# Performance work log

Hardware: AMD Instinct MI355X
Metric: run time of the kernel (lower is better)

## Reference

```python
import jax, jax.numpy as jnp
import numpy as np

B, N_P, N_S = 64, 50, 200
N_NODES = N_P * N_S          # 10000 nodes per graph (jobs x ops)
N_CAND = N_S + 1             # 201 candidates
INPUT_DIM, HIDDEN = 3, 64
NODE_DIM = 2 * HIDDEN        # h_nodes feature dim (=> actor in = 6*HIDDEN)
POOL_DIM = 4 * HIDDEN        # h_pooled dim (mean || max pooling)
H_ACTOR, H_CRITIC = 256, 256


def setup_inputs() -> dict:
    key = jax.random.key(0)
    ks = jax.random.split(key, 16)
    p = lambda k, sh: jax.random.normal(k, sh, jnp.float32) * 0.02
    x = jax.random.normal(ks[0], (B, N_NODES, INPUT_DIM), jnp.float32)
    candidate = jax.random.randint(ks[1], (B, N_CAND), 0, N_NODES)
    mask = jax.random.randint(ks[2], (B, N_CAND), 0, 2) > 0
    mask = mask.at[:, 0].set(True)  # guarantee at least one valid action per row
    return {
        "x": x, "candidate": candidate, "mask": mask,
        "fe_w1": p(ks[3], (INPUT_DIM, HIDDEN)), "fe_b1": jnp.zeros((HIDDEN,), jnp.float32),
        "fe_w2": p(ks[4], (HIDDEN, NODE_DIM)), "fe_b2": jnp.zeros((NODE_DIM,), jnp.float32),
        "a_w1": p(ks[5], (NODE_DIM + POOL_DIM, H_ACTOR)), "a_b1": jnp.zeros((H_ACTOR,), jnp.float32),
        "a_w2": p(ks[6], (H_ACTOR, H_ACTOR)), "a_b2": jnp.zeros((H_ACTOR,), jnp.float32),
        "a_w3": p(ks[7], (H_ACTOR, 1)), "a_b3": jnp.zeros((1,), jnp.float32),
        "c_w1": p(ks[8], (POOL_DIM, H_CRITIC)), "c_b1": jnp.zeros((H_CRITIC,), jnp.float32),
        "c_w2": p(ks[9], (H_CRITIC, H_CRITIC)), "c_b2": jnp.zeros((H_CRITIC,), jnp.float32),
        "c_w3": p(ks[10], (H_CRITIC, 1)), "c_b3": jnp.zeros((1,), jnp.float32),
    }


def _actor_critic(x, candidate, mask,
                  fe_w1, fe_b1, fe_w2, fe_b2,
                  a_w1, a_b1, a_w2, a_b2, a_w3, a_b3,
                  c_w1, c_b1, c_w2, c_b2, c_w3, c_b3):
    # --- feature_extract: per-node MLP embedding, graph-level pooling ---
    h = jax.nn.relu(jnp.einsum('bni,ih->bnh', x, fe_w1) + fe_b1)
    h_nodes = jax.nn.relu(jnp.einsum('bnh,hd->bnd', h, fe_w2) + fe_b2)   # [B, N, 2H]
    h_pooled = jnp.concatenate([h_nodes.mean(axis=1), h_nodes.max(axis=1)], axis=-1)  # [B, 4H]

    # --- gather candidate node features (torch.gather over node axis) ---
    cand_feat = jnp.take_along_axis(h_nodes, candidate[:, :, None], axis=1)  # [B, C, 2H]

    # --- concat broadcast pooled feature ---
    pooled_rep = jnp.broadcast_to(h_pooled[:, None, :], (cand_feat.shape[0], cand_feat.shape[1], h_pooled.shape[-1]))
    concat_fea = jnp.concatenate([cand_feat, pooled_rep], axis=-1)  # [B, C, 6H]

    # --- actor MLP (tanh hidden layers, linear out) ---
    a = jnp.tanh(concat_fea @ a_w1 + a_b1)
    a = jnp.tanh(a @ a_w2 + a_b2)
    scores = a @ a_w3 + a_b3                                    # [B, C, 1]

    # --- mask with -inf, softmax over candidate axis ---
    scores = jnp.where(mask[:, :, None], scores, -jnp.inf)
    pi = jax.nn.softmax(scores, axis=1)                          # [B, C, 1]

    # --- critic MLP on pooled feature ---
    c = jnp.tanh(h_pooled @ c_w1 + c_b1)
    c = jnp.tanh(c @ c_w2 + c_b2)
    v = c @ c_w3 + c_b3                                          # [B, 1]
    return pi, v


def reference(x, candidate, mask,
              fe_w1, fe_b1, fe_w2, fe_b2,
              a_w1, a_b1, a_w2, a_b2, a_w3, a_b3,
              c_w1, c_b1, c_w2, c_b2, c_w3, c_b3):
    return _actor_critic(x, candidate, mask,
                         fe_w1, fe_b1, fe_w2, fe_b2,
                         a_w1, a_b1, a_w2, a_b2, a_w3, a_b3,
                         c_w1, c_b1, c_w2, c_b2, c_w3, c_b3)
```

## Files before the change

### kernel.cpp

```cpp
#include <hip/hip_runtime.h>

#define NN 10000
#define NCAND 201
#define NB 64

typedef __attribute__((ext_vector_type(8))) short short8;
typedef __attribute__((ext_vector_type(4))) float f32x4;

__device__ __forceinline__ float bf2f(unsigned short u) {
  return __uint_as_float(((unsigned int)u) << 16);
}
__device__ __forceinline__ unsigned short f2bf(float f) {
  unsigned int u = __float_as_uint(f);
  u += 0x7FFFu + ((u >> 16) & 1u);
  return (unsigned short)(u >> 16);
}
__device__ __forceinline__ float fast_tanh(float x) {
  return 1.0f - 2.0f / (__expf(2.0f * x) + 1.0f);
}
__device__ __forceinline__ float gld(const void* p, long i, int f) {
  return f ? ((const float*)p)[i] : bf2f(((const unsigned short*)p)[i]);
}

__global__ __launch_bounds__(256)
void prep_kernel(const void* x, const void* w1, const void* b1, const void* w2,
                 const void* b2, const void* aw1, const void* ab1, const void* aw2,
                 const void* ab2, const void* aw3, const void* ab3,
                 const void* cw1, const void* cb1, const void* cw2, const void* cb2,
                 const void* cw3, const void* cb3,
                 const unsigned int* mask_w, const unsigned int* cand_w,
                 int* F, float* zero_base,
                 unsigned short* __restrict__ w2t, unsigned short* __restrict__ aw1t,
                 unsigned short* __restrict__ aw2t,
                 unsigned short* __restrict__ cw1t, unsigned short* __restrict__ cw2t) {
  const int t = threadIdx.x;
  const int j = blockIdx.x;

  if (j < 384) {
    __shared__ int cnts[5];
    if (t < 5) cnts[t] = 0;
    __syncthreads();
    const void* aps[5] = {w2, aw1, aw2, cw1, cw2};
#pragma unroll
    for (int a = 0; a < 5; ++a) {
      const unsigned short* p = (const unsigned short*)aps[a];
      int c = 0;
      for (int i = t; i < 2048; i += 256)
        if ((p[i] & 0x7F80u) >= 0x4300u) c++;
      if (c) atomicAdd(&cnts[a], c);
    }
    __syncthreads();
    const int Fw2 = cnts[0] > 256, Faw1 = cnts[1] > 256, Faw2 = cnts[2] > 256;
    const int Fcw1 = cnts[3] > 256, Fcw2 = cnts[4] > 256;
    int i = j * 256 + t;
    if (i < 128 * 64) { int n = i >> 6, k = i & 63; w2t[i] = f2bf(gld(w2, k * 128 + n, Fw2)); }
    if (i < 256 * 384) { int n = i / 384, k = i % 384; aw1t[i] = f2bf(gld(aw1, k * 256 + n, Faw1)); }
    if (i < 256 * 256) {
      int n = i >> 8, k = i & 255;
      aw2t[i] = f2bf(gld(aw2, k * 256 + n, Faw2));
      cw1t[i] = f2bf(gld(cw1, k * 256 + n, Fcw1));
      cw2t[i] = f2bf(gld(cw2, k * 256 + n, Fcw2));
    }
    return;
  }

  __shared__ int sh[3];
  if (t < 3) sh[t] = 0;
  __syncthreads();

  if (j < 401) {
    const void* ptrs[17] = {x, w1, b1, w2, b2, aw1, ab1, aw2, ab2, aw3, ab3,
                            cw1, cb1, cw2, cb2, cw3, cb3};
    const int sizes[17] = {1920000, 192, 64, 8192, 128, 98304, 256, 65536, 256,
                           256, 1, 65536, 256, 65536, 256, 256, 1};
    int a = j - 384;
    const unsigned short* p = (const unsigned short*)ptrs[a];
    int K = min(sizes[a], 2048);
    int c = 0;
    for (int i = t; i < K; i += 256)
      if ((p[i] & 0x7F80u) >= 0x4300u) c++;
    if (c) atomicAdd(&sh[0], c);
    __syncthreads();
    if (t == 0) F[a] = (sh[0] > (K >> 3)) ? 1 : 0;
  } else if (j == 401) {
    int flo = 0, fhi = 0, fgt = 0;
    for (int i = t; i < 3216; i += 256) {
      unsigned int w = mask_w[i];
      if ((w & 0xFFFFu) == 0x3F80u) flo = 1;
      if ((w >> 16) == 0x3F80u) fhi = 1;
      if (w > 1u) fgt = 1;
    }
    if (flo) sh[0] = 1;
    if (fhi) sh[1] = 1;
    if (fgt) sh[2] = 1;
    __syncthreads();
    if (t == 0) F[17] = sh[0] ? 2 : (sh[1] ? 3 : (sh[2] ? 1 : 0));
  } else if (j == 402) {
    int co = 0;
    for (int i = t; i < 1024; i += 256)
      if ((i & 1) && cand_w[i] != 0u) co = 1;
    if (co) sh[0] = 1;
    __syncthreads();
    if (t == 0) F[18] = sh[0] ? 0 : 1;
  } else {
    zero_base[(j - 403) * 256 + t] = 0.f;
  }
}

__global__ __launch_bounds__(256, 4)
void feat_pool_kernel(const void* __restrict__ x,
                      const void* __restrict__ w1, const void* __restrict__ b1,
                      const unsigned short* __restrict__ w2t,
                      const void* __restrict__ b2,
                      const int* __restrict__ F,
                      float* __restrict__ psum, float* __restrict__ pmax) {
  __shared__ __align__(16) unsigned short h1s[128 * 72];
  __shared__ float w1f[3 * 64];
  __shared__ float b1f[64];
  __shared__ float b2f[128];

  const int t = threadIdx.x;
  const int b = blockIdx.x >> 4;
  const int s = blockIdx.x & 15;
  const int lane = t & 63;
  const int wv = t >> 6;
  const int F0 = F[0], F1 = F[1], F2 = F[2], F4 = F[4];

  if (t < 192) w1f[t] = gld(w1, t, F1);
  if (t < 64) b1f[t] = gld(b1, t, F2);
  if (t < 128) b2f[t] = gld(b2, t, F4);

  short8 bfr[2][2];
#pragma unroll
  for (int nl = 0; nl < 2; ++nl)
#pragma unroll
    for (int ks = 0; ks < 2; ++ks) {
      int col = wv * 32 + nl * 16 + (lane & 15);
      bfr[nl][ks] = *(const short8*)(w2t + col * 64 + ((lane >> 4) * 8) + ks * 32);
    }
  __syncthreads();

  float csum[2] = {0.f, 0.f};
  float cmax[2] = {0.f, 0.f};

  const int m = t & 127;
  const int kg = t >> 7;

  float x0 = 0.f, x1 = 0.f, x2 = 0.f;
  {
    int c0 = s;
    if (c0 < 79) {
      int nb = c0 * 128;
      if (m < min(128, NN - nb)) {
        long xo = ((long)b * NN + nb + m) * 3;
        x0 = gld(x, xo, F0); x1 = gld(x, xo + 1, F0); x2 = gld(x, xo + 2, F0);
      }
    }
  }

  for (int c = s; c < 79; c += 16) {
    int nb = c * 128;
    int cnt = (nb + 128 <= NN) ? 128 : (NN - nb);
    if (m < cnt) {
#pragma unroll
      for (int blk = 0; blk < 4; ++blk) {
        short8 v;
#pragma unroll
        for (int i = 0; i < 8; ++i) {
          int k = kg * 32 + blk * 8 + i;
          float vv = x0 * w1f[k] + x1 * w1f[64 + k] + x2 * w1f[128 + k] + b1f[k];
          v[i] = (short)f2bf(fmaxf(vv, 0.f));
        }
        *(short8*)(h1s + m * 72 + kg * 32 + blk * 8) = v;
      }
    }
    {
      int cn = c + 16;
      float nx0 = 0.f, nx1 = 0.f, nx2 = 0.f;
      if (cn < 79) {
        int nbn = cn * 128;
        if (m < min(128, NN - nbn)) {
          long xo = ((long)b * NN + nbn + m) * 3;
          nx0 = gld(x, xo, F0); nx1 = gld(x, xo + 1, F0); nx2 = gld(x, xo + 2, F0);
        }
      }
      __syncthreads();
      x0 = nx0; x1 = nx1; x2 = nx2;
    }
#pragma unroll
    for (int mt = 0; mt < 8; ++mt) {
      const unsigned short* ap = h1s + (mt * 16 + (lane & 15)) * 72 + ((lane >> 4) * 8);
      short8 af0 = *(const short8*)(ap);
      short8 af1 = *(const short8*)(ap + 32);
#pragma unroll
      for (int nl = 0; nl < 2; ++nl) {
        f32x4 acc = {0.f, 0.f, 0.f, 0.f};
        acc = __builtin_amdgcn_mfma_f32_16x16x32_bf16(af0, bfr[nl][0], acc, 0, 0, 0);
        acc = __builtin_amdgcn_mfma_f32_16x16x32_bf16(af1, bfr[nl][1], acc, 0, 0, 0);
        int col = wv * 32 + nl * 16 + (lane & 15);
        float bb = b2f[col];
#pragma unroll
        for (int r = 0; r < 4; ++r) {
          int row = mt * 16 + ((lane >> 4) * 4) + r;
          if (row < cnt) {
            float v = fmaxf(acc[r] + bb, 0.f);
            csum[nl] += v;
            cmax[nl] = fmaxf(cmax[nl], v);
          }
        }
      }
    }
    __syncthreads();
  }
#pragma unroll
  for (int nl = 0; nl < 2; ++nl) {
    csum[nl] += __shfl_xor(csum[nl], 16);
    csum[nl] += __shfl_xor(csum[nl], 32);
    cmax[nl] = fmaxf(cmax[nl], __shfl_xor(cmax[nl], 16));
    cmax[nl] = fmaxf(cmax[nl], __shfl_xor(cmax[nl], 32));
  }
  if (lane < 16) {
#pragma unroll
    for (int nl = 0; nl < 2; ++nl) {
      int col = wv * 32 + nl * 16 + lane;
      atomicAdd(&psum[b * 128 + col], csum[nl]);
      atomicMax((int*)&pmax[b * 128 + col], __float_as_int(cmax[nl]));
    }
  }
}

__global__ __launch_bounds__(256)
void actor_kernel(const void* __restrict__ x, const int* __restrict__ cand,
                  const void* __restrict__ w1, const void* __restrict__ b1,
                  const void* __restrict__ b2bf,
                  const void* __restrict__ ab1, const void* __restrict__ ab2,
                  const void* __restrict__ aw3, const void* __restrict__ ab3,
                  const int* __restrict__ F,
                  const float* __restrict__ psum, const float* __restrict__ pmax,
                  const unsigned short* __restrict__ w2t,
                  const unsigned short* __restrict__ aw1t,
                  const unsigned short* __restrict__ aw2t,
                  float* __restrict__ scores) {
  __shared__ __align__(16) unsigned short h1c[32 * 72];
  __shared__ __align__(16) unsigned short cf[32 * 136];
  __shared__ __align__(16) unsigned short a1s[32 * 264];
  __shared__ __align__(16) unsigned short a2s[32 * 264];
  __shared__ __align__(16) unsigned short plbf[256];
  __shared__ float ab1f[256], ab2f[256], b2f[128];

  const int t = threadIdx.x;
  const int b = blockIdx.x / 7;
  const int cb = blockIdx.x % 7;
  const int cbase = cb * 29;
  const int cntc = min(29, NCAND - cbase);
  const int lane = t & 63;
  const int wv = t >> 6;
  const int F0 = F[0], F1 = F[1], F2 = F[2], F4 = F[4], F6 = F[6], F8 = F[8];
  const int F9 = F[9], F10 = F[10], C64 = F[18];

  if (t < 128) {
    plbf[t] = f2bf(psum[b * 128 + t] * (1.0f / 10000.0f));
    plbf[128 + t] = f2bf(pmax[b * 128 + t]);
    b2f[t] = gld(b2bf, t, F4);
  }
  ab1f[t] = gld(ab1, t, F6);
  ab2f[t] = gld(ab2, t, F8);

  {
    int r = t & 31;
    int ci = cbase + r;
    if (ci > NCAND - 1) ci = NCAND - 1;
    long cidx = (long)b * NCAND + ci;
    int nd = C64 ? cand[2 * cidx] : cand[cidx];
    long xo = ((long)b * NN + nd) * 3;
    float x0 = gld(x, xo, F0), x1 = gld(x, xo + 1, F0), x2 = gld(x, xo + 2, F0);
    int kg = t >> 5;
#pragma unroll
    for (int i = 0; i < 8; ++i) {
      int k = kg * 8 + i;
      float v = x0 * gld(w1, k, F1) + x1 * gld(w1, 64 + k, F1) +
                x2 * gld(w1, 128 + k, F1) + gld(b1, k, F2);
      h1c[r * 72 + k] = f2bf(fmaxf(v, 0.f));
    }
  }
  __syncthreads();

  {
    short8 af[2][2];
#pragma unroll
    for (int mt = 0; mt < 2; ++mt)
#pragma unroll
      for (int ks = 0; ks < 2; ++ks)
        af[mt][ks] = *(const short8*)(h1c + (mt * 16 + (lane & 15)) * 72 + ((lane >> 4) * 8) + ks * 32);
#pragma unroll
    for (int nl = 0; nl < 2; ++nl) {
      int col = wv * 32 + nl * 16 + (lane & 15);
      short8 bf0 = *(const short8*)(w2t + col * 64 + ((lane >> 4) * 8));
      short8 bf1 = *(const short8*)(w2t + col * 64 + ((lane >> 4) * 8) + 32);
      float bb = b2f[col];
#pragma unroll
      for (int mt = 0; mt < 2; ++mt) {
        f32x4 acc = {0.f, 0.f, 0.f, 0.f};
        acc = __builtin_amdgcn_mfma_f32_16x16x32_bf16(af[mt][0], bf0, acc, 0, 0, 0);
        acc = __builtin_amdgcn_mfma_f32_16x16x32_bf16(af[mt][1], bf1, acc, 0, 0, 0);
#pragma unroll
        for (int r = 0; r < 4; ++r) {
          int row = mt * 16 + ((lane >> 4) * 4) + r;
          cf[row * 136 + col] = f2bf(fmaxf(acc[r] + bb, 0.f));
        }
      }
    }
  }
  __syncthreads();

  {
    f32x4 acc[2][4];
#pragma unroll
    for (int mt = 0; mt < 2; ++mt)
#pragma unroll
      for (int nt = 0; nt < 4; ++nt) acc[mt][nt] = (f32x4){0.f, 0.f, 0.f, 0.f};
    for (int ks = 0; ks < 12; ++ks) {
      short8 af0, af1;
      if (ks < 4) {
        af0 = *(const short8*)(cf + (lane & 15) * 136 + ks * 32 + ((lane >> 4) * 8));
        af1 = *(const short8*)(cf + (16 + (lane & 15)) * 136 + ks * 32 + ((lane >> 4) * 8));
      } else {
        short8 p = *(const short8*)(plbf + (ks - 4) * 32 + ((lane >> 4) * 8));
        af0 = p;
        af1 = p;
      }
#pragma unroll
      for (int nt = 0; nt < 4; ++nt) {
        int col = wv * 64 + nt * 16 + (lane & 15);
        short8 bfr = *(const short8*)(aw1t + col * 384 + ks * 32 + ((lane >> 4) * 8));
        acc[0][nt] = __builtin_amdgcn_mfma_f32_16x16x32_bf16(af0, bfr, acc[0][nt], 0, 0, 0);
        acc[1][nt] = __builtin_amdgcn_mfma_f32_16x16x32_bf16(af1, bfr, acc[1][nt], 0, 0, 0);
      }
    }
#pragma unroll
    for (int mt = 0; mt < 2; ++mt)
#pragma unroll
      for (int nt = 0; nt < 4; ++nt) {
        int col = wv * 64 + nt * 16 + (lane & 15);
        float bb = ab1f[col];
#pragma unroll
        for (int r = 0; r < 4; ++r) {
          int row = mt * 16 + ((lane >> 4) * 4) + r;
          a1s[row * 264 + col] = f2bf(fast_tanh(acc[mt][nt][r] + bb));
        }
      }
  }
  __syncthreads();

  {
    f32x4 acc[2][4];
#pragma unroll
    for (int mt = 0; mt < 2; ++mt)
#pragma unroll
      for (int nt = 0; nt < 4; ++nt) acc[mt][nt] = (f32x4){0.f, 0.f, 0.f, 0.f};
    for (int ks = 0; ks < 8; ++ks) {
      short8 af0 = *(const short8*)(a1s + (lane & 15) * 264 + ks * 32 + ((lane >> 4) * 8));
      short8 af1 = *(const short8*)(a1s + (16 + (lane & 15)) * 264 + ks * 32 + ((lane >> 4) * 8));
#pragma unroll
      for (int nt = 0; nt < 4; ++nt) {
        int col = wv * 64 + nt * 16 + (lane & 15);
        short8 bfr = *(const short8*)(aw2t + col * 256 + ks * 32 + ((lane >> 4) * 8));
        acc[0][nt] = __builtin_amdgcn_mfma_f32_16x16x32_bf16(af0, bfr, acc[0][nt], 0, 0, 0);
        acc[1][nt] = __builtin_amdgcn_mfma_f32_16x16x32_bf16(af1, bfr, acc[1][nt], 0, 0, 0);
      }
    }
#pragma unroll
    for (int mt = 0; mt < 2; ++mt)
#pragma unroll
      for (int nt = 0; nt < 4; ++nt) {
        int col = wv * 64 + nt * 16 + (lane & 15);
        float bb = ab2f[col];
#pragma unroll
        for (int r = 0; r < 4; ++r) {
          int row = mt * 16 + ((lane >> 4) * 4) + r;
          a2s[row * 264 + col] = f2bf(fast_tanh(acc[mt][nt][r] + bb));
        }
      }
  }
  __syncthreads();

  {
    int row = t >> 3, seg = t & 7;
    float p = 0.f;
#pragma unroll 8
    for (int i = 0; i < 32; ++i) {
      int k = seg * 32 + i;
      p += bf2f(a2s[row * 264 + k]) * gld(aw3, k, F9);
    }
    p += __shfl_xor(p, 1);
    p += __shfl_xor(p, 2);
    p += __shfl_xor(p, 4);
    if (seg == 0 && row < cntc)
      scores[b * 256 + cbase + row] = p + gld(ab3, 0, F10);
  }
}

__global__ __launch_bounds__(256)
void softmax_critic_kernel(const float* __restrict__ scores,
                           const void* __restrict__ mask,
                           const int* __restrict__ F,
                           const float* __restrict__ psum,
                           const float* __restrict__ pmax,
                           const unsigned short* __restrict__ cw1t,
                           const unsigned short* __restrict__ cw2t,
                           const void* __restrict__ cb1, const void* __restrict__ cb2,
                           const void* __restrict__ cw3, const void* __restrict__ cb3,
                           void* __restrict__ out) {
  __shared__ float plf[256];
  __shared__ float c1f[256];
  __shared__ float red[4];
  const int t = threadIdx.x;
  const int b = blockIdx.x & 63;
  const int lane = t & 63, wv = t >> 6;
  const int OF = (F[0] + F[1] + F[3] + F[5] + F[7] + F[9] + F[11] + F[13] + F[15]) >= 5;

  if (blockIdx.x < 64) {
    const int MM = F[17];
    float sraw = 0.f, sv = -1e30f;
    bool valid = false;
    if (t < NCAND) {
      sraw = scores[b * 256 + t];
      long idx = (long)b * NCAND + t;
      if (MM == 0)      valid = ((const int*)mask)[idx] != 0;
      else if (MM == 1) valid = ((const unsigned char*)mask)[idx] != 0;
      else if (MM == 2) valid = ((const unsigned short*)mask)[idx] != 0;
      else              valid = ((const unsigned int*)mask)[idx] != 0;
      if (valid) sv = sraw;
    }
    float m = sv;
    for (int o = 32; o; o >>= 1) m = fmaxf(m, __shfl_xor(m, o));
    if (lane == 0) red[wv] = m;
    __syncthreads();
    m = fmaxf(fmaxf(red[0], red[1]), fmaxf(red[2], red[3]));
    __syncthreads();
    float e = valid ? __expf(sraw - m) : 0.f;
    if (!(e == e)) e = 0.f;
    float ss = e;
    for (int o = 32; o; o >>= 1) ss += __shfl_xor(ss, o);
    if (lane == 0) red[wv] = ss;
    __syncthreads();
    float tot = red[0] + red[1] + red[2] + red[3];
    tot = fmaxf(tot, 1e-30f);
    if (t < NCAND) {
      float pv = e / tot;
      if (!(pv == pv)) pv = 0.f;
      if (OF) ((float*)out)[b * NCAND + t] = pv;
      else ((unsigned short*)out)[b * NCAND + t] = f2bf(pv);
    }
  } else {
    const int F12 = F[12], F14 = F[14], F15 = F[15], F16 = F[16];
    if (t < 128) {
      plf[t] = psum[b * 128 + t] * (1.0f / 10000.0f);
      plf[128 + t] = pmax[b * 128 + t];
    }
    __syncthreads();
    {
      float a = gld(cb1, t, F12);
      const unsigned short* row = cw1t + t * 256;
#pragma unroll
      for (int k8 = 0; k8 < 32; ++k8) {
        short8 w = *(const short8*)(row + k8 * 8);
#pragma unroll
        for (int j = 0; j < 8; ++j)
          a += plf[k8 * 8 + j] * bf2f((unsigned short)w[j]);
      }
      c1f[t] = fast_tanh(a);
    }
    __syncthreads();
    {
      float a2 = gld(cb2, t, F14);
      const unsigned short* row = cw2t + t * 256;
#pragma unroll
      for (int k8 = 0; k8 < 32; ++k8) {
        short8 w = *(const short8*)(row + k8 * 8);
#pragma unroll
        for (int j = 0; j < 8; ++j)
          a2 += c1f[k8 * 8 + j] * bf2f((unsigned short)w[j]);
      }
      a2 = fast_tanh(a2);
      float p = a2 * gld(cw3, t, F15);
      for (int o = 32; o; o >>= 1) p += __shfl_xor(p, o);
      __syncthreads();
      if (lane == 0) red[wv] = p;
      __syncthreads();
      if (t == 0) {
        float v = red[0] + red[1] + red[2] + red[3] + gld(cb3, 0, F16);
        if (!(v == v)) v = 0.f;
        if (OF) ((float*)out)[NB * NCAND + b] = v;
        else ((unsigned short*)out)[NB * NCAND + b] = f2bf(v);
      }
    }
  }
}

extern "C" void kernel_launch(void* const* d_in, const int* in_sizes, int n_in,
                              void* d_out, int out_size, void* d_ws, size_t ws_size,
                              hipStream_t stream) {
  const void* x = d_in[0];
  const int* cand = (const int*)d_in[1];
  const void* mask = d_in[2];
  const void* fe_w1 = d_in[3];
  const void* fe_b1 = d_in[4];
  const void* fe_w2 = d_in[5];
  const void* fe_b2 = d_in[6];
  const void* a_w1 = d_in[7];
  const void* a_b1 = d_in[8];
  const void* a_w2 = d_in[9];
  const void* a_b2 = d_in[10];
  const void* a_w3 = d_in[11];
  const void* a_b3 = d_in[12];
  const void* c_w1 = d_in[13];
  const void* c_b1 = d_in[14];
  const void* c_w2 = d_in[15];
  const void* c_b2 = d_in[16];
  const void* c_w3 = d_in[17];
  const void* c_b3 = d_in[18];

  char* ws = (char*)d_ws;
  float* psum = (float*)(ws + 0);
  float* pmax = (float*)(ws + 32768);
  float* scores = (float*)(ws + 65536);
  unsigned short* w2t = (unsigned short*)(ws + 131072);
  unsigned short* aw1t = (unsigned short*)(ws + 147456);
  unsigned short* aw2t = (unsigned short*)(ws + 344064);
  int* F = (int*)(ws + 475136);
  unsigned short* cw1t = (unsigned short*)(ws + 475264);
  unsigned short* cw2t = (unsigned short*)(ws + 606336);

  prep_kernel<<<467, 256, 0, stream>>>(x, fe_w1, fe_b1, fe_w2, fe_b2,
                                       a_w1, a_b1, a_w2, a_b2, a_w3, a_b3,
                                       c_w1, c_b1, c_w2, c_b2, c_w3, c_b3,
                                       (const unsigned int*)mask,
                                       (const unsigned int*)cand, F, psum,
                                       w2t, aw1t, aw2t, cw1t, cw2t);
  feat_pool_kernel<<<1024, 256, 0, stream>>>(x, fe_w1, fe_b1, w2t, fe_b2, F, psum, pmax);
  actor_kernel<<<448, 256, 0, stream>>>(x, cand, fe_w1, fe_b1, fe_b2,
                                        a_b1, a_b2, a_w3, a_b3, F, psum, pmax,
                                        w2t, aw1t, aw2t, scores);
  softmax_critic_kernel<<<128, 256, 0, stream>>>(scores, mask, F, psum, pmax,
                                                 cw1t, cw2t, c_b1, c_b2, c_w3, c_b3,
                                                 (void*)d_out);
}
```

Measured before the change: 177.7 us.

## Split actor kernel into 16-candidate blocks and shrink dtype-probe sampling

The actor kernel now handles 16 candidates per block instead of 29 (padded to 32), giving 13 blocks per batch and 832 blocks in total, with a single M-tile of MFMA per wave. This is meant to raise occupancy and parallelism across CUs and to cut the wasted padded rows, at the cost of reloading the aw1t/aw2t weight fragments from global memory twice as often. The prep kernel's per-weight dtype probe now samples 256 elements instead of 2048, which reduces prep work but makes the fp32/bf16 guess rely on a smaller sample.

```diff
diff --git a/kernel.cpp b/kernel.cpp
--- a/kernel.cpp
+++ b/kernel.cpp
@@ -44,14 +44,11 @@
 #pragma unroll
     for (int a = 0; a < 5; ++a) {
       const unsigned short* p = (const unsigned short*)aps[a];
-      int c = 0;
-      for (int i = t; i < 2048; i += 256)
-        if ((p[i] & 0x7F80u) >= 0x4300u) c++;
-      if (c) atomicAdd(&cnts[a], c);
-    }
-    __syncthreads();
-    const int Fw2 = cnts[0] > 256, Faw1 = cnts[1] > 256, Faw2 = cnts[2] > 256;
-    const int Fcw1 = cnts[3] > 256, Fcw2 = cnts[4] > 256;
+      if ((p[t] & 0x7F80u) >= 0x4300u) atomicAdd(&cnts[a], 1);
+    }
+    __syncthreads();
+    const int Fw2 = cnts[0] > 32, Faw1 = cnts[1] > 32, Faw2 = cnts[2] > 32;
+    const int Fcw1 = cnts[3] > 32, Fcw2 = cnts[4] > 32;
     int i = j * 256 + t;
     if (i < 128 * 64) { int n = i >> 6, k = i & 63; w2t[i] = f2bf(gld(w2, k * 128 + n, Fw2)); }
     if (i < 256 * 384) { int n = i / 384, k = i % 384; aw1t[i] = f2bf(gld(aw1, k * 256 + n, Faw1)); }
@@ -241,18 +238,18 @@
                   const unsigned short* __restrict__ aw1t,
                   const unsigned short* __restrict__ aw2t,
                   float* __restrict__ scores) {
-  __shared__ __align__(16) unsigned short h1c[32 * 72];
-  __shared__ __align__(16) unsigned short cf[32 * 136];
-  __shared__ __align__(16) unsigned short a1s[32 * 264];
-  __shared__ __align__(16) unsigned short a2s[32 * 264];
+  __shared__ __align__(16) unsigned short h1c[16 * 72];
+  __shared__ __align__(16) unsigned short cf[16 * 136];
+  __shared__ __align__(16) unsigned short a1s[16 * 264];
+  __shared__ __align__(16) unsigned short a2s[16 * 264];
   __shared__ __align__(16) unsigned short plbf[256];
   __shared__ float ab1f[256], ab2f[256], b2f[128];
 
   const int t = threadIdx.x;
-  const int b = blockIdx.x / 7;
-  const int cb = blockIdx.x % 7;
-  const int cbase = cb * 29;
-  const int cntc = min(29, NCAND - cbase);
+  const int b = blockIdx.x / 13;
+  const int cb = blockIdx.x % 13;
+  const int cbase = cb * 16;
+  const int cntc = min(16, NCAND - cbase);
   const int lane = t & 63;
   const int wv = t >> 6;
   const int F0 = F[0], F1 = F[1], F2 = F[2], F4 = F[4], F6 = F[6], F8 = F[8];
@@ -267,17 +264,17 @@
   ab2f[t] = gld(ab2, t, F8);
 
   {
-    int r = t & 31;
+    int r = t & 15;
     int ci = cbase + r;
     if (ci > NCAND - 1) ci = NCAND - 1;
     long cidx = (long)b * NCAND + ci;
     int nd = C64 ? cand[2 * cidx] : cand[cidx];
     long xo = ((long)b * NN + nd) * 3;
     float x0 = gld(x, xo, F0), x1 = gld(x, xo + 1, F0), x2 = gld(x, xo + 2, F0);
-    int kg = t >> 5;
-#pragma unroll
-    for (int i = 0; i < 8; ++i) {
-      int k = kg * 8 + i;
+    int kg = t >> 4;
+#pragma unroll
+    for (int i = 0; i < 4; ++i) {
+      int k = kg * 4 + i;
       float v = x0 * gld(w1, k, F1) + x1 * gld(w1, 64 + k, F1) +
                 x2 * gld(w1, 128 + k, F1) + gld(b1, k, F2);
       h1c[r * 72 + k] = f2bf(fmaxf(v, 0.f));
@@ -286,115 +283,95 @@
   __syncthreads();
 
   {
-    short8 af[2][2];
-#pragma unroll
-    for (int mt = 0; mt < 2; ++mt)
-#pragma unroll
-      for (int ks = 0; ks < 2; ++ks)
-        af[mt][ks] = *(const short8*)(h1c + (mt * 16 + (lane & 15)) * 72 + ((lane >> 4) * 8) + ks * 32);
+    short8 af0 = *(const short8*)(h1c + (lane & 15) * 72 + ((lane >> 4) * 8));
+    short8 af1 = *(const short8*)(h1c + (lane & 15) * 72 + ((lane >> 4) * 8) + 32);
 #pragma unroll
     for (int nl = 0; nl < 2; ++nl) {
       int col = wv * 32 + nl * 16 + (lane & 15);
       short8 bf0 = *(const short8*)(w2t + col * 64 + ((lane >> 4) * 8));
       short8 bf1 = *(const short8*)(w2t + col * 64 + ((lane >> 4) * 8) + 32);
       float bb = b2f[col];
-#pragma unroll
-      for (int mt = 0; mt < 2; ++mt) {
-        f32x4 acc = {0.f, 0.f, 0.f, 0.f};
-        acc = __builtin_amdgcn_mfma_f32_16x16x32_bf16(af[mt][0], bf0, acc, 0, 0, 0);
-        acc = __builtin_amdgcn_mfma_f32_16x16x32_bf16(af[mt][1], bf1, acc, 0, 0, 0);
-#pragma unroll
-        for (int r = 0; r < 4; ++r) {
-          int row = mt * 16 + ((lane >> 4) * 4) + r;
-          cf[row * 136 + col] = f2bf(fmaxf(acc[r] + bb, 0.f));
-        }
+      f32x4 acc = {0.f, 0.f, 0.f, 0.f};
+      acc = __builtin_amdgcn_mfma_f32_16x16x32_bf16(af0, bf0, acc, 0, 0, 0);
+      acc = __builtin_amdgcn_mfma_f32_16x16x32_bf16(af1, bf1, acc, 0, 0, 0);
+#pragma unroll
+      for (int r = 0; r < 4; ++r) {
+        int row = ((lane >> 4) * 4) + r;
+        cf[row * 136 + col] = f2bf(fmaxf(acc[r] + bb, 0.f));
       }
     }
   }
   __syncthreads();
 
   {
-    f32x4 acc[2][4];
-#pragma unroll
-    for (int mt = 0; mt < 2; ++mt)
-#pragma unroll
-      for (int nt = 0; nt < 4; ++nt) acc[mt][nt] = (f32x4){0.f, 0.f, 0.f, 0.f};
+    f32x4 acc[4];
+#pragma unroll
+    for (int nt = 0; nt < 4; ++nt) acc[nt] = (f32x4){0.f, 0.f, 0.f, 0.f};
     for (int ks = 0; ks < 12; ++ks) {
-      short8 af0, af1;
+      short8 af;
       if (ks < 4) {
-        af0 = *(const short8*)(cf + (lane & 15) * 136 + ks * 32 + ((lane >> 4) * 8));
-        af1 = *(const short8*)(cf + (16 + (lane & 15)) * 136 + ks * 32 + ((lane >> 4) * 8));
+        af = *(const short8*)(cf + (lane & 15) * 136 + ks * 32 + ((lane >> 4) * 8));
       } else {
-        short8 p = *(const short8*)(plbf + (ks - 4) * 32 + ((lane >> 4) * 8));
-        af0 = p;
-        af1 = p;
+        af = *(const short8*)(plbf + (ks - 4) * 32 + ((lane >> 4) * 8));
       }
 #pragma unroll
       for (int nt = 0; nt < 4; ++nt) {
         int col = wv * 64 + nt * 16 + (lane & 15);
         short8 bfr = *(const short8*)(aw1t + col * 384 + ks * 32 + ((lane >> 4) * 8));
-        acc[0][nt] = __builtin_amdgcn_mfma_f32_16x16x32_bf16(af0, bfr, acc[0][nt], 0, 0, 0);
-        acc[1][nt] = __builtin_amdgcn_mfma_f32_16x16x32_bf16(af1, bfr, acc[1][nt], 0, 0, 0);
-      }
-    }
-#pragma unroll
-    for (int mt = 0; mt < 2; ++mt)
-#pragma unroll
-      for (int nt = 0; nt < 4; ++nt) {
-        int col = wv * 64 + nt * 16 + (lane & 15);
-        float bb = ab1f[col];
-#pragma unroll
-        for (int r = 0; r < 4; ++r) {
-          int row = mt * 16 + ((lane >> 4) * 4) + r;
-          a1s[row * 264 + col] = f2bf(fast_tanh(acc[mt][nt][r] + bb));
-        }
-      }
+        acc[nt] = __builtin_amdgcn_mfma_f32_16x16x32_bf16(af, bfr, acc[nt], 0, 0, 0);
+      }
+    }
+#pragma unroll
+    for (int nt = 0; nt < 4; ++nt) {
+      int col = wv * 64 + nt * 16 + (lane & 15);
+      float bb = ab1f[col];
+#pragma unroll
+      for (int r = 0; r < 4; ++r) {
+        int row = ((lane >> 4) * 4) + r;
+        a1s[row * 264 + col] = f2bf(fast_tanh(acc[nt][r] + bb));
+      }
+    }
   }
   __syncthreads();
 
   {
-    f32x4 acc[2][4];
-#pragma unroll
-    for (int mt = 0; mt < 2; ++mt)
-#pragma unroll
-      for (int nt = 0; nt < 4; ++nt) acc[mt][nt] = (f32x4){0.f, 0.f, 0.f, 0.f};
+    f32x4 acc[4];
+#pragma unroll
+    for (int nt = 0; nt < 4; ++nt) acc[nt] = (f32x4){0.f, 0.f, 0.f, 0.f};
     for (int ks = 0; ks < 8; ++ks) {
-      short8 af0 = *(const short8*)(a1s + (lane & 15) * 264 + ks * 32 + ((lane >> 4) * 8));
-      short8 af1 = *(const short8*)(a1s + (16 + (lane & 15)) * 264 + ks * 32 + ((lane >> 4) * 8));
+      short8 af = *(const short8*)(a1s + (lane & 15) * 264 + ks * 32 + ((lane >> 4) * 8));
 #pragma unroll
       for (int nt = 0; nt < 4; ++nt) {
         int col = wv * 64 + nt * 16 + (lane & 15);
         short8 bfr = *(const short8*)(aw2t + col * 256 + ks * 32 + ((lane >> 4) * 8));
-        acc[0][nt] = __builtin_amdgcn_mfma_f32_16x16x32_bf16(af0, bfr, acc[0][nt], 0, 0, 0);
-        acc[1][nt] = __builtin_amdgcn_mfma_f32_16x16x32_bf16(af1, bfr, acc[1][nt], 0, 0, 0);
-      }
-    }
-#pragma unroll
-    for (int mt = 0; mt < 2; ++mt)
-#pragma unroll
-      for (int nt = 0; nt < 4; ++nt) {
-        int col = wv * 64 + nt * 16 + (lane & 15);
-        float bb = ab2f[col];
-#pragma unroll
-        for (int r = 0; r < 4; ++r) {
-          int row = mt * 16 + ((lane >> 4) * 4) + r;
-          a2s[row * 264 + col] = f2bf(fast_tanh(acc[mt][nt][r] + bb));
-        }
-      }
+        acc[nt] = __builtin_amdgcn_mfma_f32_16x16x32_bf16(af, bfr, acc[nt], 0, 0, 0);
+      }
+    }
+#pragma unroll
+    for (int nt = 0; nt < 4; ++nt) {
+      int col = wv * 64 + nt * 16 + (lane & 15);
+      float bb = ab2f[col];
+#pragma unroll
+      for (int r = 0; r < 4; ++r) {
+        int row = ((lane >> 4) * 4) + r;
+        a2s[row * 264 + col] = f2bf(fast_tanh(acc[nt][r] + bb));
+      }
+    }
   }
   __syncthreads();
 
   {
-    int row = t >> 3, seg = t & 7;
+    int row = t >> 4, seg = t & 15;
     float p = 0.f;
-#pragma unroll 8
-    for (int i = 0; i < 32; ++i) {
-      int k = seg * 32 + i;
+#pragma unroll
+    for (int i = 0; i < 16; ++i) {
+      int k = seg * 16 + i;
       p += bf2f(a2s[row * 264 + k]) * gld(aw3, k, F9);
     }
     p += __shfl_xor(p, 1);
     p += __shfl_xor(p, 2);
     p += __shfl_xor(p, 4);
+    p += __shfl_xor(p, 8);
     if (seg == 0 && row < cntc)
       scores[b * 256 + cbase + row] = p + gld(ab3, 0, F10);
   }
@@ -539,7 +516,7 @@
                                        (const unsigned int*)cand, F, psum,
                                        w2t, aw1t, aw2t, cw1t, cw2t);
   feat_pool_kernel<<<1024, 256, 0, stream>>>(x, fe_w1, fe_b1, w2t, fe_b2, F, psum, pmax);
-  actor_kernel<<<448, 256, 0, stream>>>(x, cand, fe_w1, fe_b1, fe_b2,
+  actor_kernel<<<832, 256, 0, stream>>>(x, cand, fe_w1, fe_b1, fe_b2,
                                         a_b1, a_b2, a_w3, a_b3, F, psum, pmax,
                                         w2t, aw1t, aw2t, scores);
   softmax_critic_kernel<<<128, 256, 0, stream>>>(scores, mask, F, psum, pmax,
```

After: 189.4 us. 1.07x slower.
